# Kernel tuning notes

Measured on AMD Instinct MI355X. Metric: run time of the kernel, lower is better.

## Reference

```python
import jax, jax.numpy as jnp
import numpy as np

N_NODES = 20000
N_EDGES = 640000
D = 128
H = 256


def setup_inputs() -> dict:
    key = jax.random.key(0)
    ks = jax.random.split(key, 8)
    s = lambda fan_in: 1.0 / np.sqrt(fan_in)
    return {
        "nf": jax.random.normal(ks[0], (N_NODES, D), jnp.float32),
        "ef": jax.random.normal(ks[1], (N_EDGES, D), jnp.float32),
        "src": jax.random.randint(ks[2], (N_EDGES,), 0, N_NODES, jnp.int32),
        "dst": jax.random.randint(ks[3], (N_EDGES,), 0, N_NODES, jnp.int32),
        "We1": jax.random.normal(ks[4], (3 * D, H), jnp.float32) * s(3 * D),
        "be1": jnp.zeros((H,), jnp.float32),
        "We2": jax.random.normal(ks[5], (H, D), jnp.float32) * s(H),
        "be2": jnp.zeros((D,), jnp.float32),
        "Wn1": jax.random.normal(ks[6], (2 * D, H), jnp.float32) * s(2 * D),
        "bn1": jnp.zeros((H,), jnp.float32),
        "Wn2": jax.random.normal(ks[7], (H, D), jnp.float32) * s(H),
        "bn2": jnp.zeros((D,), jnp.float32),
    }


def reference(nf, ef, src, dst, We1, be1, We2, be2, Wn1, bn1, Wn2, bn2):
    # edge update: concat [ef, sender_nf, receiver_nf] -> MLP
    em_in = jnp.concatenate([ef, nf[src], nf[dst]], axis=-1)  # [E, 3D]
    h = jax.nn.relu(em_in @ We1 + be1)
    updated_ef = h @ We2 + be2  # [E, D]
    # message = copy_e('h'); aggregate = segment sum at destination nodes
    agg_m = jax.ops.segment_sum(updated_ef, dst, num_segments=nf.shape[0])  # [N, D]
    # node update: concat [agg_m, nf] -> MLP
    nm_in = jnp.concatenate([agg_m, nf], axis=-1)  # [N, 2D]
    hn = jax.nn.relu(nm_in @ Wn1 + bn1)
    updated_nf = hn @ Wn2 + bn2  # [N, D]
    return updated_nf, updated_ef
```

## Files before the change

kernel.cpp:

```cpp
#include <hip/hip_runtime.h>
#include <hip/hip_bf16.h>

#define N_NODES 20000
#define N_EDGES 640000
#define D 128
#define H 256

using bf16x8 = __attribute__((ext_vector_type(8))) short;
using f32x4  = __attribute__((ext_vector_type(4))) float;

__device__ __forceinline__ unsigned short f2bf(float f) {
  unsigned int u = __float_as_uint(f);
  unsigned int r = u + 0x7fffu + ((u >> 16) & 1u);
  return (unsigned short)(r >> 16);
}

__device__ __forceinline__ void gload_lds16(const void* g, void* l) {
  __builtin_amdgcn_global_load_lds(
      (const __attribute__((address_space(1))) void*)g,
      (__attribute__((address_space(3))) void*)l, 16, 0, 0);
}

__global__ __launch_bounds__(256) void prep_kernel(
    const float* __restrict__ nf, const int* __restrict__ dst,
    const float* __restrict__ We1, const float* __restrict__ We2,
    const float* __restrict__ Wn1, const float* __restrict__ Wn2,
    unsigned short* __restrict__ nf_bf, unsigned short* __restrict__ We1F,
    unsigned short* __restrict__ We2F, unsigned short* __restrict__ Wn1T,
    unsigned short* __restrict__ Wn2T, int* __restrict__ deg) {
  int idx = blockIdx.x * 256 + threadIdx.x;
  if (idx < N_NODES * D) {
    nf_bf[idx] = f2bf(nf[idx]);
  }
  if (idx < N_EDGES) {
    atomicAdd(&deg[dst[idx]], 1);
  }
  if (idx < 98304) {
    int e = idx & 7, l = (idx >> 3) & 63, nt = (idx >> 9) & 15, ks = idx >> 13;
    int k = ks * 32 + (l >> 4) * 8 + e;
    int col = nt * 16 + (l & 15);
    We1F[idx] = f2bf(We1[k * 256 + col]);
  } else if (idx < 131072) {
    int j = idx - 98304;
    int e = j & 7, l = (j >> 3) & 63, nt = (j >> 9) & 7, ks = j >> 12;
    int k = ks * 32 + (l >> 4) * 8 + e;
    int col = nt * 16 + (l & 15);
    We2F[j] = f2bf(We2[k * 128 + col]);
  } else if (idx < 196608) {
    int j = idx - 131072; int n = j / 256, k = j % 256;
    Wn1T[j] = f2bf(Wn1[k * 256 + n]);
  } else if (idx < 229376) {
    int j = idx - 196608; int n = j / 256, k = j % 256;
    Wn2T[j] = f2bf(Wn2[k * 128 + n]);
  }
}

__global__ __launch_bounds__(1024) void scan_kernel(const int* __restrict__ deg,
                                                    int* __restrict__ cursor) {
  __shared__ int sums[1024];
  const int t = threadIdx.x;
  const int base = t * 20;
  int local[20];
  int s = 0;
#pragma unroll
  for (int i = 0; i < 20; i++) {
    int p = base + i;
    int v = (p < N_NODES) ? deg[p] : 0;
    local[i] = s;
    s += v;
  }
  sums[t] = s;
  __syncthreads();
  for (int ofs = 1; ofs < 1024; ofs <<= 1) {
    int v = (t >= ofs) ? sums[t - ofs] : 0;
    __syncthreads();
    sums[t] += v;
    __syncthreads();
  }
  int ebase = sums[t] - s;
#pragma unroll
  for (int i = 0; i < 20; i++) {
    int p = base + i;
    if (p < N_NODES) cursor[p] = ebase + local[i];
  }
}

__global__ __launch_bounds__(256) void fill_kernel(const int* __restrict__ dst,
                                                   int* __restrict__ cursor,
                                                   int* __restrict__ eidx) {
  int e = blockIdx.x * 256 + threadIdx.x;
  if (e < N_EDGES) {
    int d = dst[e];
    int pos = atomicAdd(&cursor[d], 1);
    eidx[pos] = e;
  }
}

#define HS 264

__global__ __launch_bounds__(512, 6) void edge_kernel(
    const float* __restrict__ ef, const unsigned short* __restrict__ nf_bf,
    const int* __restrict__ src, const int* __restrict__ dst,
    const unsigned short* __restrict__ We1F, const float* __restrict__ be1,
    const unsigned short* __restrict__ We2F, const float* __restrict__ be2,
    float* __restrict__ out_ef) {
  __shared__ unsigned short smemA[64 * 384];
  unsigned short* hbuf = smemA;

  const int tid  = threadIdx.x;
  const int lane = tid & 63;
  const int w    = tid >> 6;
  const int ln15 = lane & 15;
  const int q    = lane >> 4;
  const int wr   = w >> 2;
  const int wc   = w & 3;
  const int e0   = blockIdx.x * 64;

  {
#pragma unroll
    for (int i = 0; i < 2; i++) {
      int id = w * 2 + i;
      int ksub = id >> 2, mt = id & 3;
      int sidx = src[e0 + mt * 16 + ln15];
      gload_lds16(&nf_bf[(size_t)sidx * 128 + ksub * 32 + q * 8],
                  &smemA[((4 + ksub) * 4 + mt) * 512]);
    }
#pragma unroll
    for (int i = 0; i < 2; i++) {
      int id = w * 2 + i;
      int ksub = id >> 2, mt = id & 3;
      int didx = dst[e0 + mt * 16 + ln15];
      gload_lds16(&nf_bf[(size_t)didx * 128 + ksub * 32 + q * 8],
                  &smemA[((8 + ksub) * 4 + mt) * 512]);
    }
#pragma unroll
    for (int i = 0; i < 2; i++) {
      int id = w * 2 + i;
      int kse = id >> 2, mt = id & 3;
      const float* p = &ef[(size_t)(e0 + mt * 16 + ln15) * 128 + kse * 32 + q * 8];
      float4 v0 = *(const float4*)p;
      float4 v1 = *(const float4*)(p + 4);
      uint4 o;
      o.x = (unsigned)f2bf(v0.x) | ((unsigned)f2bf(v0.y) << 16);
      o.y = (unsigned)f2bf(v0.z) | ((unsigned)f2bf(v0.w) << 16);
      o.z = (unsigned)f2bf(v1.x) | ((unsigned)f2bf(v1.y) << 16);
      o.w = (unsigned)f2bf(v1.z) | ((unsigned)f2bf(v1.w) << 16);
      *(uint4*)&smemA[(kse * 4 + mt) * 512 + lane * 8] = o;
    }
  }
  __syncthreads();

  f32x4 acc[2][4] = {};
#pragma unroll
  for (int ks = 0; ks < 12; ks++) {
    bf16x8 a[2], b[4];
#pragma unroll
    for (int m = 0; m < 2; m++)
      a[m] = *(const bf16x8*)&smemA[(ks * 4 + wr * 2 + m) * 512 + lane * 8];
#pragma unroll
    for (int nt = 0; nt < 4; nt++)
      b[nt] = *(const bf16x8*)&We1F[(size_t)((ks * 16 + wc * 4 + nt) * 64 + lane) * 8];
#pragma unroll
    for (int m = 0; m < 2; m++)
#pragma unroll
      for (int nt = 0; nt < 4; nt++)
        acc[m][nt] = __builtin_amdgcn_mfma_f32_16x16x32_bf16(a[m], b[nt], acc[m][nt], 0, 0, 0);
  }

  float bias1[4];
#pragma unroll
  for (int nt = 0; nt < 4; nt++) bias1[nt] = be1[wc * 64 + nt * 16 + ln15];

  __syncthreads();

#pragma unroll
  for (int m = 0; m < 2; m++)
#pragma unroll
    for (int nt = 0; nt < 4; nt++)
#pragma unroll
      for (int r = 0; r < 4; r++) {
        float v = acc[m][nt][r] + bias1[nt];
        v = v > 0.f ? v : 0.f;
        hbuf[(wr * 32 + m * 16 + q * 4 + r) * HS + wc * 64 + nt * 16 + ln15] = f2bf(v);
      }
  __syncthreads();

  f32x4 acc2[2][2] = {};
#pragma unroll
  for (int ks = 0; ks < 8; ks++) {
    bf16x8 a2[2], b2[2];
#pragma unroll
    for (int m = 0; m < 2; m++)
      a2[m] = *(const bf16x8*)&hbuf[(wr * 32 + m * 16 + ln15) * HS + ks * 32 + q * 8];
#pragma unroll
    for (int nt = 0; nt < 2; nt++)
      b2[nt] = *(const bf16x8*)&We2F[(size_t)((ks * 8 + wc * 2 + nt) * 64 + lane) * 8];
#pragma unroll
    for (int m = 0; m < 2; m++)
#pragma unroll
      for (int nt = 0; nt < 2; nt++)
        acc2[m][nt] = __builtin_amdgcn_mfma_f32_16x16x32_bf16(a2[m], b2[nt], acc2[m][nt], 0, 0, 0);
  }

  float bias2[2];
#pragma unroll
  for (int nt = 0; nt < 2; nt++) bias2[nt] = be2[wc * 32 + nt * 16 + ln15];

#pragma unroll
  for (int m = 0; m < 2; m++) {
#pragma unroll
    for (int r = 0; r < 4; r++) {
      int e = e0 + wr * 32 + m * 16 + q * 4 + r;
#pragma unroll
      for (int nt = 0; nt < 2; nt++) {
        int col = wc * 32 + nt * 16 + ln15;
        out_ef[(size_t)e * 128 + col] = acc2[m][nt][r] + bias2[nt];
      }
    }
  }
}

__global__ __launch_bounds__(256) void agg_kernel(
    const float* __restrict__ out_ef, const int* __restrict__ cursor,
    const int* __restrict__ eidx, unsigned short* __restrict__ agg_bf) {
  const int lane = threadIdx.x & 63;
  const int wave = threadIdx.x >> 6;
  const int node = blockIdx.x * 4 + wave;
  if (node >= N_NODES) return;

  const float2* ef2 = (const float2*)out_ef;
  int s = (node == 0) ? 0 : cursor[node - 1];
  int t = cursor[node];
  float a0x=0.f,a0y=0.f,a1x=0.f,a1y=0.f,a2x=0.f,a2y=0.f,a3x=0.f,a3y=0.f;
  int j = s;
  for (; j + 8 <= t; j += 8) {
    int e0v=eidx[j],   e1v=eidx[j+1], e2v=eidx[j+2], e3v=eidx[j+3];
    int e4v=eidx[j+4], e5v=eidx[j+5], e6v=eidx[j+6], e7v=eidx[j+7];
    float2 v0=ef2[(size_t)e0v*64+lane], v1=ef2[(size_t)e1v*64+lane];
    float2 v2=ef2[(size_t)e2v*64+lane], v3=ef2[(size_t)e3v*64+lane];
    float2 v4=ef2[(size_t)e4v*64+lane], v5=ef2[(size_t)e5v*64+lane];
    float2 v6=ef2[(size_t)e6v*64+lane], v7=ef2[(size_t)e7v*64+lane];
    a0x+=v0.x+v4.x; a0y+=v0.y+v4.y;
    a1x+=v1.x+v5.x; a1y+=v1.y+v5.y;
    a2x+=v2.x+v6.x; a2y+=v2.y+v6.y;
    a3x+=v3.x+v7.x; a3y+=v3.y+v7.y;
  }
  for (; j < t; ++j) {
    int ev = eidx[j];
    float2 v = ef2[(size_t)ev*64+lane];
    a0x += v.x; a0y += v.y;
  }
  float ax = (a0x + a1x) + (a2x + a3x);
  float ay = (a0y + a1y) + (a2y + a3y);
  unsigned int packed = (unsigned int)f2bf(ax) | ((unsigned int)f2bf(ay) << 16);
  *(unsigned int*)&agg_bf[(size_t)node * 128 + 2 * lane] = packed;
}

__global__ __launch_bounds__(256, 3) void node_kernel(
    const unsigned short* __restrict__ agg_bf, const unsigned short* __restrict__ nf_bf,
    const unsigned short* __restrict__ Wn1T, const float* __restrict__ bn1,
    const unsigned short* __restrict__ Wn2T, const float* __restrict__ bn2,
    float* __restrict__ out_nf) {
  __shared__ unsigned short smem[64 * HS];

  const int tid  = threadIdx.x;
  const int lane = tid & 63;
  const int wave = tid >> 6;
  const int ln15 = lane & 15;
  const int q    = lane >> 4;
  const int n0   = blockIdx.x * 64;

  const int nb1 = wave * 64;
  const int nb2 = wave * 32;

  float bias1[4];
#pragma unroll
  for (int nt = 0; nt < 4; nt++) bias1[nt] = bn1[nb1 + nt * 16 + ln15];

  {
#pragma unroll
    for (int i = 0; i < 4; i++) {
      int flat = tid + 256 * i;
      int row = flat >> 4, seg = flat & 15;
      int node = n0 + row;
      uint4 va = make_uint4(0u, 0u, 0u, 0u);
      uint4 vn = make_uint4(0u, 0u, 0u, 0u);
      if (node < N_NODES) {
        va = *(const uint4*)&agg_bf[(size_t)node * 128 + seg * 8];
        vn = *(const uint4*)&nf_bf[(size_t)node * 128 + seg * 8];
      }
      *(uint4*)&smem[row * HS + seg * 8] = va;
      *(uint4*)&smem[row * HS + 128 + seg * 8] = vn;
    }
  }
  __syncthreads();

  f32x4 acc[4][4] = {};
#pragma unroll
  for (int ks = 0; ks < 8; ks++) {
    const int kc = ks * 32 + q * 8;
    bf16x8 a[4], b[4];
#pragma unroll
    for (int mt = 0; mt < 4; mt++)
      a[mt] = *(const bf16x8*)&smem[(mt * 16 + ln15) * HS + kc];
#pragma unroll
    for (int nt = 0; nt < 4; nt++)
      b[nt] = *(const bf16x8*)&Wn1T[(size_t)(nb1 + nt * 16 + ln15) * 256 + kc];
#pragma unroll
    for (int mt = 0; mt < 4; mt++)
#pragma unroll
      for (int nt = 0; nt < 4; nt++)
        acc[mt][nt] = __builtin_amdgcn_mfma_f32_16x16x32_bf16(a[mt], b[nt], acc[mt][nt], 0, 0, 0);
  }

  float bias2[2];
#pragma unroll
  for (int nt = 0; nt < 2; nt++) bias2[nt] = bn2[nb2 + nt * 16 + ln15];

  __syncthreads();

#pragma unroll
  for (int mt = 0; mt < 4; mt++)
#pragma unroll
    for (int nt = 0; nt < 4; nt++)
#pragma unroll
      for (int r = 0; r < 4; r++) {
        float v = acc[mt][nt][r] + bias1[nt];
        v = v > 0.f ? v : 0.f;
        smem[(mt * 16 + q * 4 + r) * HS + nb1 + nt * 16 + ln15] = f2bf(v);
      }
  __syncthreads();

  f32x4 acc2[4][2] = {};
#pragma unroll
  for (int ks = 0; ks < 8; ks++) {
    const int kc = ks * 32 + q * 8;
    bf16x8 a2[4], b2[2];
#pragma unroll
    for (int mt = 0; mt < 4; mt++)
      a2[mt] = *(const bf16x8*)&smem[(mt * 16 + ln15) * HS + kc];
#pragma unroll
    for (int nt = 0; nt < 2; nt++)
      b2[nt] = *(const bf16x8*)&Wn2T[(size_t)(nb2 + nt * 16 + ln15) * 256 + kc];
#pragma unroll
    for (int mt = 0; mt < 4; mt++)
#pragma unroll
      for (int nt = 0; nt < 2; nt++)
        acc2[mt][nt] = __builtin_amdgcn_mfma_f32_16x16x32_bf16(a2[mt], b2[nt], acc2[mt][nt], 0, 0, 0);
  }

#pragma unroll
  for (int mt = 0; mt < 4; mt++) {
#pragma unroll
    for (int r = 0; r < 4; r++) {
      int row = mt * 16 + q * 4 + r;
      int node = n0 + row;
      if (node < N_NODES) {
#pragma unroll
        for (int nt = 0; nt < 2; nt++) {
          int col = nb2 + nt * 16 + ln15;
          out_nf[(size_t)node * 128 + col] = acc2[mt][nt][r] + bias2[nt];
        }
      }
    }
  }
}

extern "C" void kernel_launch(void* const* d_in, const int* in_sizes, int n_in,
                              void* d_out, int out_size, void* d_ws, size_t ws_size,
                              hipStream_t stream) {
  const float* nf  = (const float*)d_in[0];
  const float* ef  = (const float*)d_in[1];
  const int*   src = (const int*)d_in[2];
  const int*   dst = (const int*)d_in[3];
  const float* We1 = (const float*)d_in[4];
  const float* be1 = (const float*)d_in[5];
  const float* We2 = (const float*)d_in[6];
  const float* be2 = (const float*)d_in[7];
  const float* Wn1 = (const float*)d_in[8];
  const float* bn1 = (const float*)d_in[9];
  const float* Wn2 = (const float*)d_in[10];
  const float* bn2 = (const float*)d_in[11];

  float* out_nf = (float*)d_out;
  float* out_ef = out_nf + (size_t)N_NODES * D;

  char* ws = (char*)d_ws;
  unsigned short* nf_bf  = (unsigned short*)ws;
  unsigned short* We1F   = (unsigned short*)(ws + 5120000);
  unsigned short* We2F   = (unsigned short*)(ws + 5316608);
  unsigned short* Wn1T   = (unsigned short*)(ws + 5382144);
  unsigned short* Wn2T   = (unsigned short*)(ws + 5513216);
  int*            deg    = (int*)(ws + 5578752);
  int*            cursor = (int*)(ws + 5658752);
  int*            eidx   = (int*)(ws + 5738752);
  unsigned short* agg_bf = (unsigned short*)(ws + 8298752);

  hipMemsetAsync(deg, 0, N_NODES * sizeof(int), stream);
  prep_kernel<<<10000, 256, 0, stream>>>(nf, dst, We1, We2, Wn1, Wn2,
                                         nf_bf, We1F, We2F, Wn1T, Wn2T, deg);
  scan_kernel<<<1, 1024, 0, stream>>>(deg, cursor);
  fill_kernel<<<N_EDGES / 256, 256, 0, stream>>>(dst, cursor, eidx);
  edge_kernel<<<N_EDGES / 64, 512, 0, stream>>>(ef, nf_bf, src, dst,
                                                We1F, be1, We2F, be2, out_ef);
  agg_kernel<<<N_NODES / 4, 256, 0, stream>>>(out_ef, cursor, eidx, agg_bf);
  node_kernel<<<(N_NODES + 63) / 64, 256, 0, stream>>>(agg_bf, nf_bf,
                                                       Wn1T, bn1, Wn2T, bn2, out_nf);
}
```

Measured before the change: 914.0 us.

## Fuse segment-sum aggregation into edge kernel via dst-sorted edge order and atomics

The edge kernel now processes edges in destination-sorted order through eidx. It gathers ef, src and dst indirectly, scatters out_ef to the original edge positions, and reduces runs of equal destination inside the tile before atomically adding into an fp32 aggregate buffer. The separate agg_kernel pass that re-read all edge outputs is removed, and the node kernel converts the fp32 aggregate to bf16 when loading it. In exchange the ef reads and out_ef writes become scattered rather than contiguous, and there are float atomics plus extra syncs and a zero-init of a 10MB buffer.

Result: no change. 921.6 us (+0.8%).

```diff
diff --git a/kernel.cpp b/kernel.cpp
--- a/kernel.cpp
+++ b/kernel.cpp
@@ -25,11 +25,13 @@
     const float* __restrict__ nf, const int* __restrict__ dst,
     const float* __restrict__ We1, const float* __restrict__ We2,
     const float* __restrict__ Wn1, const float* __restrict__ Wn2,
-    unsigned short* __restrict__ nf_bf, unsigned short* __restrict__ We1F,
-    unsigned short* __restrict__ We2F, unsigned short* __restrict__ Wn1T,
-    unsigned short* __restrict__ Wn2T, int* __restrict__ deg) {
+    float* __restrict__ agg, unsigned short* __restrict__ nf_bf,
+    unsigned short* __restrict__ We1F, unsigned short* __restrict__ We2F,
+    unsigned short* __restrict__ Wn1T, unsigned short* __restrict__ Wn2T,
+    int* __restrict__ deg) {
   int idx = blockIdx.x * 256 + threadIdx.x;
   if (idx < N_NODES * D) {
+    agg[idx] = 0.f;
     nf_bf[idx] = f2bf(nf[idx]);
   }
   if (idx < N_EDGES) {
@@ -97,15 +99,20 @@
 }
 
 #define HS 264
+#define CF 132
 
 __global__ __launch_bounds__(512, 6) void edge_kernel(
     const float* __restrict__ ef, const unsigned short* __restrict__ nf_bf,
     const int* __restrict__ src, const int* __restrict__ dst,
+    const int* __restrict__ eidx,
     const unsigned short* __restrict__ We1F, const float* __restrict__ be1,
     const unsigned short* __restrict__ We2F, const float* __restrict__ be2,
-    float* __restrict__ out_ef) {
+    float* __restrict__ out_ef, float* __restrict__ agg) {
   __shared__ unsigned short smemA[64 * 384];
+  __shared__ int smemE[64];
+  __shared__ int smemD[64];
   unsigned short* hbuf = smemA;
+  float* cbuf = (float*)smemA;
 
   const int tid  = threadIdx.x;
   const int lane = tid & 63;
@@ -116,12 +123,18 @@
   const int wc   = w & 3;
   const int e0   = blockIdx.x * 64;
 
+  if (tid < 64) {
+    int e = eidx[e0 + tid];
+    smemE[tid] = e;
+    smemD[tid] = dst[e];
+  }
   {
 #pragma unroll
     for (int i = 0; i < 2; i++) {
       int id = w * 2 + i;
       int ksub = id >> 2, mt = id & 3;
-      int sidx = src[e0 + mt * 16 + ln15];
+      int e = eidx[e0 + mt * 16 + ln15];
+      int sidx = src[e];
       gload_lds16(&nf_bf[(size_t)sidx * 128 + ksub * 32 + q * 8],
                   &smemA[((4 + ksub) * 4 + mt) * 512]);
     }
@@ -129,7 +142,8 @@
     for (int i = 0; i < 2; i++) {
       int id = w * 2 + i;
       int ksub = id >> 2, mt = id & 3;
-      int didx = dst[e0 + mt * 16 + ln15];
+      int e = eidx[e0 + mt * 16 + ln15];
+      int didx = dst[e];
       gload_lds16(&nf_bf[(size_t)didx * 128 + ksub * 32 + q * 8],
                   &smemA[((8 + ksub) * 4 + mt) * 512]);
     }
@@ -137,7 +151,8 @@
     for (int i = 0; i < 2; i++) {
       int id = w * 2 + i;
       int kse = id >> 2, mt = id & 3;
-      const float* p = &ef[(size_t)(e0 + mt * 16 + ln15) * 128 + kse * 32 + q * 8];
+      int e = eidx[e0 + mt * 16 + ln15];
+      const float* p = &ef[(size_t)e * 128 + kse * 32 + q * 8];
       float4 v0 = *(const float4*)p;
       float4 v1 = *(const float4*)(p + 4);
       uint4 o;
@@ -206,58 +221,45 @@
 #pragma unroll
   for (int nt = 0; nt < 2; nt++) bias2[nt] = be2[wc * 32 + nt * 16 + ln15];
 
+  __syncthreads();
+
 #pragma unroll
   for (int m = 0; m < 2; m++) {
 #pragma unroll
     for (int r = 0; r < 4; r++) {
-      int e = e0 + wr * 32 + m * 16 + q * 4 + r;
+      int row = wr * 32 + m * 16 + q * 4 + r;
+      int e = smemE[row];
 #pragma unroll
       for (int nt = 0; nt < 2; nt++) {
         int col = wc * 32 + nt * 16 + ln15;
-        out_ef[(size_t)e * 128 + col] = acc2[m][nt][r] + bias2[nt];
+        float v = acc2[m][nt][r] + bias2[nt];
+        out_ef[(size_t)e * 128 + col] = v;
+        cbuf[row * CF + col] = v;
       }
     }
   }
-}
-
-__global__ __launch_bounds__(256) void agg_kernel(
-    const float* __restrict__ out_ef, const int* __restrict__ cursor,
-    const int* __restrict__ eidx, unsigned short* __restrict__ agg_bf) {
-  const int lane = threadIdx.x & 63;
-  const int wave = threadIdx.x >> 6;
-  const int node = blockIdx.x * 4 + wave;
-  if (node >= N_NODES) return;
-
-  const float2* ef2 = (const float2*)out_ef;
-  int s = (node == 0) ? 0 : cursor[node - 1];
-  int t = cursor[node];
-  float a0x=0.f,a0y=0.f,a1x=0.f,a1y=0.f,a2x=0.f,a2y=0.f,a3x=0.f,a3y=0.f;
-  int j = s;
-  for (; j + 8 <= t; j += 8) {
-    int e0v=eidx[j],   e1v=eidx[j+1], e2v=eidx[j+2], e3v=eidx[j+3];
-    int e4v=eidx[j+4], e5v=eidx[j+5], e6v=eidx[j+6], e7v=eidx[j+7];
-    float2 v0=ef2[(size_t)e0v*64+lane], v1=ef2[(size_t)e1v*64+lane];
-    float2 v2=ef2[(size_t)e2v*64+lane], v3=ef2[(size_t)e3v*64+lane];
-    float2 v4=ef2[(size_t)e4v*64+lane], v5=ef2[(size_t)e5v*64+lane];
-    float2 v6=ef2[(size_t)e6v*64+lane], v7=ef2[(size_t)e7v*64+lane];
-    a0x+=v0.x+v4.x; a0y+=v0.y+v4.y;
-    a1x+=v1.x+v5.x; a1y+=v1.y+v5.y;
-    a2x+=v2.x+v6.x; a2y+=v2.y+v6.y;
-    a3x+=v3.x+v7.x; a3y+=v3.y+v7.y;
-  }
-  for (; j < t; ++j) {
-    int ev = eidx[j];
-    float2 v = ef2[(size_t)ev*64+lane];
-    a0x += v.x; a0y += v.y;
-  }
-  float ax = (a0x + a1x) + (a2x + a3x);
-  float ay = (a0y + a1y) + (a2y + a3y);
-  unsigned int packed = (unsigned int)f2bf(ax) | ((unsigned int)f2bf(ay) << 16);
-  *(unsigned int*)&agg_bf[(size_t)node * 128 + 2 * lane] = packed;
+  __syncthreads();
+
+  {
+    const int col = tid & 127;
+    const int r0  = (tid >> 7) * 16;
+    float s = 0.f;
+    int dcur = smemD[r0];
+    for (int r = r0; r < r0 + 16; ++r) {
+      int dn = smemD[r];
+      float v = cbuf[r * CF + col];
+      if (dn != dcur) {
+        atomicAdd(&agg[(size_t)dcur * 128 + col], s);
+        s = 0.f; dcur = dn;
+      }
+      s += v;
+    }
+    atomicAdd(&agg[(size_t)dcur * 128 + col], s);
+  }
 }
 
 __global__ __launch_bounds__(256, 3) void node_kernel(
-    const unsigned short* __restrict__ agg_bf, const unsigned short* __restrict__ nf_bf,
+    const float* __restrict__ agg, const unsigned short* __restrict__ nf_bf,
     const unsigned short* __restrict__ Wn1T, const float* __restrict__ bn1,
     const unsigned short* __restrict__ Wn2T, const float* __restrict__ bn2,
     float* __restrict__ out_nf) {
@@ -278,18 +280,24 @@
   for (int nt = 0; nt < 4; nt++) bias1[nt] = bn1[nb1 + nt * 16 + ln15];
 
   {
+    const float4* agg4 = (const float4*)agg;
+#pragma unroll
+    for (int i = 0; i < 8; i++) {
+      int flat = tid + 256 * i;
+      int row = flat >> 5, c4 = flat & 31;
+      int node = n0 + row;
+      float4 v = make_float4(0.f, 0.f, 0.f, 0.f);
+      if (node < N_NODES) v = agg4[(size_t)node * 32 + c4];
+      ushort4 o = { f2bf(v.x), f2bf(v.y), f2bf(v.z), f2bf(v.w) };
+      *(ushort4*)&smem[row * HS + c4 * 4] = o;
+    }
 #pragma unroll
     for (int i = 0; i < 4; i++) {
       int flat = tid + 256 * i;
       int row = flat >> 4, seg = flat & 15;
       int node = n0 + row;
-      uint4 va = make_uint4(0u, 0u, 0u, 0u);
       uint4 vn = make_uint4(0u, 0u, 0u, 0u);
-      if (node < N_NODES) {
-        va = *(const uint4*)&agg_bf[(size_t)node * 128 + seg * 8];
-        vn = *(const uint4*)&nf_bf[(size_t)node * 128 + seg * 8];
-      }
-      *(uint4*)&smem[row * HS + seg * 8] = va;
+      if (node < N_NODES) vn = *(const uint4*)&nf_bf[(size_t)node * 128 + seg * 8];
       *(uint4*)&smem[row * HS + 128 + seg * 8] = vn;
     }
   }
@@ -394,16 +402,15 @@
   int*            deg    = (int*)(ws + 5578752);
   int*            cursor = (int*)(ws + 5658752);
   int*            eidx   = (int*)(ws + 5738752);
-  unsigned short* agg_bf = (unsigned short*)(ws + 8298752);
+  float*          agg    = (float*)(ws + 8298752);
 
   hipMemsetAsync(deg, 0, N_NODES * sizeof(int), stream);
   prep_kernel<<<10000, 256, 0, stream>>>(nf, dst, We1, We2, Wn1, Wn2,
-                                         nf_bf, We1F, We2F, Wn1T, Wn2T, deg);
+                                         agg, nf_bf, We1F, We2F, Wn1T, Wn2T, deg);
   scan_kernel<<<1, 1024, 0, stream>>>(deg, cursor);
   fill_kernel<<<N_EDGES / 256, 256, 0, stream>>>(dst, cursor, eidx);
-  edge_kernel<<<N_EDGES / 64, 512, 0, stream>>>(ef, nf_bf, src, dst,
-                                                We1F, be1, We2F, be2, out_ef);
-  agg_kernel<<<N_NODES / 4, 256, 0, stream>>>(out_ef, cursor, eidx, agg_bf);
-  node_kernel<<<(N_NODES + 63) / 64, 256, 0, stream>>>(agg_bf, nf_bf,
+  edge_kernel<<<N_EDGES / 64, 512, 0, stream>>>(ef, nf_bf, src, dst, eidx,
+                                                We1F, be1, We2F, be2, out_ef, agg);
+  node_kernel<<<(N_NODES + 63) / 64, 256, 0, stream>>>(agg, nf_bf,
                                                        Wn1T, bn1, Wn2T, bn2, out_nf);
 }
```

## Precompute per-node projections of sender/receiver features before edge MLP

Applied to the files above, without the earlier changes.

Splits the first edge-layer matmul algebraically: nf@We1_src and nf@We1_dst (plus bias) are computed once per node in a new pgemm kernel and stored as bf16. The edge kernel then gathers and sums the two 256-wide projected rows instead of gathering raw node features and doing the 256-deep K portion per edge, cutting edge-kernel MFMA work to a third for layer 1. In exchange, gathered bytes per edge double (two 512B rows instead of two 256B rows), and extra bf16 rounding of the partial sums adds error.

New measurement: 869.7 us. -4.8%, faster.

```diff
diff --git a/kernel.cpp b/kernel.cpp
--- a/kernel.cpp
+++ b/kernel.cpp
@@ -13,6 +13,14 @@
   unsigned int u = __float_as_uint(f);
   unsigned int r = u + 0x7fffu + ((u >> 16) & 1u);
   return (unsigned short)(r >> 16);
+}
+__device__ __forceinline__ float bf2f(unsigned short u) {
+  return __uint_as_float(((unsigned int)u) << 16);
+}
+__device__ __forceinline__ unsigned int pksum(unsigned int a, unsigned int b) {
+  float lo = bf2f((unsigned short)(a & 0xffff)) + bf2f((unsigned short)(b & 0xffff));
+  float hi = bf2f((unsigned short)(a >> 16))    + bf2f((unsigned short)(b >> 16));
+  return (unsigned int)f2bf(lo) | ((unsigned int)f2bf(hi) << 16);
 }
 
 __device__ __forceinline__ void gload_lds16(const void* g, void* l) {
@@ -96,16 +104,83 @@
   }
 }
 
+__global__ __launch_bounds__(512, 4) void pgemm_kernel(
+    const unsigned short* __restrict__ nf_bf, const unsigned short* __restrict__ We1F,
+    const float* __restrict__ be1,
+    unsigned short* __restrict__ Ps, unsigned short* __restrict__ Pd) {
+  __shared__ unsigned short smem[16 * 512];
+
+  const int tid  = threadIdx.x;
+  const int lane = tid & 63;
+  const int w    = tid >> 6;
+  const int ln15 = lane & 15;
+  const int q    = lane >> 4;
+  const int wr   = w >> 2;
+  const int wc   = w & 3;
+  const int n0   = blockIdx.x * 64;
+
+#pragma unroll
+  for (int i = 0; i < 2; i++) {
+    int id = w * 2 + i;
+    int ksub = id >> 2, mt = id & 3;
+    int node = n0 + mt * 16 + ln15;
+    if (node >= N_NODES) node = N_NODES - 1;
+    gload_lds16(&nf_bf[(size_t)node * 128 + ksub * 32 + q * 8],
+                &smem[(ksub * 4 + mt) * 512]);
+  }
+  __syncthreads();
+
+  f32x4 accs[2][4] = {};
+  f32x4 accd[2][4] = {};
+#pragma unroll
+  for (int ks = 0; ks < 4; ks++) {
+    bf16x8 a[2], bs[4], bd[4];
+#pragma unroll
+    for (int m = 0; m < 2; m++)
+      a[m] = *(const bf16x8*)&smem[(ks * 4 + wr * 2 + m) * 512 + lane * 8];
+#pragma unroll
+    for (int nt = 0; nt < 4; nt++) {
+      bs[nt] = *(const bf16x8*)&We1F[(size_t)(((4 + ks) * 16 + wc * 4 + nt) * 64 + lane) * 8];
+      bd[nt] = *(const bf16x8*)&We1F[(size_t)(((8 + ks) * 16 + wc * 4 + nt) * 64 + lane) * 8];
+    }
+#pragma unroll
+    for (int m = 0; m < 2; m++)
+#pragma unroll
+      for (int nt = 0; nt < 4; nt++) {
+        accs[m][nt] = __builtin_amdgcn_mfma_f32_16x16x32_bf16(a[m], bs[nt], accs[m][nt], 0, 0, 0);
+        accd[m][nt] = __builtin_amdgcn_mfma_f32_16x16x32_bf16(a[m], bd[nt], accd[m][nt], 0, 0, 0);
+      }
+  }
+
+#pragma unroll
+  for (int m = 0; m < 2; m++) {
+#pragma unroll
+    for (int r = 0; r < 4; r++) {
+      int node = n0 + wr * 32 + m * 16 + q * 4 + r;
+      if (node < N_NODES) {
+#pragma unroll
+        for (int nt = 0; nt < 4; nt++) {
+          int col = wc * 64 + nt * 16 + ln15;
+          Ps[(size_t)node * 256 + col] = f2bf(accs[m][nt][r]);
+          Pd[(size_t)node * 256 + col] = f2bf(accd[m][nt][r] + be1[col]);
+        }
+      }
+    }
+  }
+}
+
 #define HS 264
 
 __global__ __launch_bounds__(512, 6) void edge_kernel(
-    const float* __restrict__ ef, const unsigned short* __restrict__ nf_bf,
+    const float* __restrict__ ef,
+    const unsigned short* __restrict__ Ps, const unsigned short* __restrict__ Pd,
     const int* __restrict__ src, const int* __restrict__ dst,
-    const unsigned short* __restrict__ We1F, const float* __restrict__ be1,
+    const unsigned short* __restrict__ We1F,
     const unsigned short* __restrict__ We2F, const float* __restrict__ be2,
     float* __restrict__ out_ef) {
-  __shared__ unsigned short smemA[64 * 384];
-  unsigned short* hbuf = smemA;
+  __shared__ unsigned short smem[16 * 512 + 64 * HS];
+  unsigned short* efF  = smem;
+  unsigned short* pbuf = smem + 8192;
 
   const int tid  = threadIdx.x;
   const int lane = tid & 63;
@@ -117,22 +192,6 @@
   const int e0   = blockIdx.x * 64;
 
   {
-#pragma unroll
-    for (int i = 0; i < 2; i++) {
-      int id = w * 2 + i;
-      int ksub = id >> 2, mt = id & 3;
-      int sidx = src[e0 + mt * 16 + ln15];
-      gload_lds16(&nf_bf[(size_t)sidx * 128 + ksub * 32 + q * 8],
-                  &smemA[((4 + ksub) * 4 + mt) * 512]);
-    }
-#pragma unroll
-    for (int i = 0; i < 2; i++) {
-      int id = w * 2 + i;
-      int ksub = id >> 2, mt = id & 3;
-      int didx = dst[e0 + mt * 16 + ln15];
-      gload_lds16(&nf_bf[(size_t)didx * 128 + ksub * 32 + q * 8],
-                  &smemA[((8 + ksub) * 4 + mt) * 512]);
-    }
 #pragma unroll
     for (int i = 0; i < 2; i++) {
       int id = w * 2 + i;
@@ -145,18 +204,34 @@
       o.y = (unsigned)f2bf(v0.z) | ((unsigned)f2bf(v0.w) << 16);
       o.z = (unsigned)f2bf(v1.x) | ((unsigned)f2bf(v1.y) << 16);
       o.w = (unsigned)f2bf(v1.z) | ((unsigned)f2bf(v1.w) << 16);
-      *(uint4*)&smemA[(kse * 4 + mt) * 512 + lane * 8] = o;
+      *(uint4*)&efF[(kse * 4 + mt) * 512 + lane * 8] = o;
+    }
+    int prow = tid >> 3, seg = tid & 7;
+    int e = e0 + prow;
+    int s = src[e];
+    int d = dst[e];
+    const uint4* ps4 = (const uint4*)&Ps[(size_t)s * 256 + seg * 32];
+    const uint4* pd4 = (const uint4*)&Pd[(size_t)d * 256 + seg * 32];
+#pragma unroll
+    for (int i = 0; i < 4; i++) {
+      uint4 a = ps4[i], b = pd4[i];
+      uint4 o;
+      o.x = pksum(a.x, b.x);
+      o.y = pksum(a.y, b.y);
+      o.z = pksum(a.z, b.z);
+      o.w = pksum(a.w, b.w);
+      *(uint4*)&pbuf[prow * HS + seg * 32 + i * 8] = o;
     }
   }
   __syncthreads();
 
   f32x4 acc[2][4] = {};
 #pragma unroll
-  for (int ks = 0; ks < 12; ks++) {
+  for (int ks = 0; ks < 4; ks++) {
     bf16x8 a[2], b[4];
 #pragma unroll
     for (int m = 0; m < 2; m++)
-      a[m] = *(const bf16x8*)&smemA[(ks * 4 + wr * 2 + m) * 512 + lane * 8];
+      a[m] = *(const bf16x8*)&efF[(ks * 4 + wr * 2 + m) * 512 + lane * 8];
 #pragma unroll
     for (int nt = 0; nt < 4; nt++)
       b[nt] = *(const bf16x8*)&We1F[(size_t)((ks * 16 + wc * 4 + nt) * 64 + lane) * 8];
@@ -167,21 +242,16 @@
         acc[m][nt] = __builtin_amdgcn_mfma_f32_16x16x32_bf16(a[m], b[nt], acc[m][nt], 0, 0, 0);
   }
 
-  float bias1[4];
-#pragma unroll
-  for (int nt = 0; nt < 4; nt++) bias1[nt] = be1[wc * 64 + nt * 16 + ln15];
-
-  __syncthreads();
-
 #pragma unroll
   for (int m = 0; m < 2; m++)
 #pragma unroll
     for (int nt = 0; nt < 4; nt++)
 #pragma unroll
       for (int r = 0; r < 4; r++) {
-        float v = acc[m][nt][r] + bias1[nt];
+        int idx = (wr * 32 + m * 16 + q * 4 + r) * HS + wc * 64 + nt * 16 + ln15;
+        float v = acc[m][nt][r] + bf2f(pbuf[idx]);
         v = v > 0.f ? v : 0.f;
-        hbuf[(wr * 32 + m * 16 + q * 4 + r) * HS + wc * 64 + nt * 16 + ln15] = f2bf(v);
+        pbuf[idx] = f2bf(v);
       }
   __syncthreads();
 
@@ -191,7 +261,7 @@
     bf16x8 a2[2], b2[2];
 #pragma unroll
     for (int m = 0; m < 2; m++)
-      a2[m] = *(const bf16x8*)&hbuf[(wr * 32 + m * 16 + ln15) * HS + ks * 32 + q * 8];
+      a2[m] = *(const bf16x8*)&pbuf[(wr * 32 + m * 16 + ln15) * HS + ks * 32 + q * 8];
 #pragma unroll
     for (int nt = 0; nt < 2; nt++)
       b2[nt] = *(const bf16x8*)&We2F[(size_t)((ks * 8 + wc * 2 + nt) * 64 + lane) * 8];
@@ -395,14 +465,17 @@
   int*            cursor = (int*)(ws + 5658752);
   int*            eidx   = (int*)(ws + 5738752);
   unsigned short* agg_bf = (unsigned short*)(ws + 8298752);
+  unsigned short* Ps     = (unsigned short*)(ws + 13418752);
+  unsigned short* Pd     = (unsigned short*)(ws + 23658752);
 
   hipMemsetAsync(deg, 0, N_NODES * sizeof(int), stream);
   prep_kernel<<<10000, 256, 0, stream>>>(nf, dst, We1, We2, Wn1, Wn2,
                                          nf_bf, We1F, We2F, Wn1T, Wn2T, deg);
+  pgemm_kernel<<<(N_NODES + 63) / 64, 512, 0, stream>>>(nf_bf, We1F, be1, Ps, Pd);
   scan_kernel<<<1, 1024, 0, stream>>>(deg, cursor);
   fill_kernel<<<N_EDGES / 256, 256, 0, stream>>>(dst, cursor, eidx);
-  edge_kernel<<<N_EDGES / 64, 512, 0, stream>>>(ef, nf_bf, src, dst,
-                                                We1F, be1, We2F, be2, out_ef);
+  edge_kernel<<<N_EDGES / 64, 512, 0, stream>>>(ef, Ps, Pd, src, dst,
+                                                We1F, We2F, be2, out_ef);
   agg_kernel<<<N_NODES / 4, 256, 0, stream>>>(out_ef, cursor, eidx, agg_bf);
   node_kernel<<<(N_NODES + 63) / 64, 256, 0, stream>>>(agg_bf, nf_bf,
                                                        Wn1T, bn1, Wn2T, bn2, out_nf);
```
